# Performance work log

Measured on AMD Instinct MI355X. Metric: run time of the kernel, lower is better.

The kernel has to match this reference:

```python
import jax, jax.numpy as jnp
import numpy as np


def setup_inputs() -> dict:
    key = jax.random.key(0)
    ks = jax.random.split(key, 5)
    B, H, W, KV = 32, 32, 32, 1024
    N, K, V = 16, 64, 64
    return {
        "key_value": jax.random.normal(ks[0], (B, H, W, KV), dtype=jnp.float32),
        "query": jax.random.normal(ks[1], (1, 1, N, K), dtype=jnp.float32),
        "k_kernel": jax.random.normal(ks[2], (KV, N * K), dtype=jnp.float32) * 0.03,
        "k_bias": jnp.zeros((N * K,), dtype=jnp.float32),
        "v_kernel": jax.random.normal(ks[3], (KV, N * V), dtype=jnp.float32) * 0.03,
        "v_bias": jnp.zeros((N * V,), dtype=jnp.float32),
    }


def reference(key_value, query, k_kernel, k_bias, v_kernel, v_bias):
    # key_value: [B,H,W,KV]; 1x1 conv == channel GEMM
    B, H, W, KV = key_value.shape
    N, K = query.shape[2], query.shape[3]
    V = v_kernel.shape[1] // N
    x = key_value.reshape(B, H * W, KV)                      # [B,HW,KV]
    k = (x @ k_kernel + k_bias).reshape(B, H * W, N, K)       # [B,HW,N,K]
    v = (x @ v_kernel + v_bias).reshape(B, H * W, N, V)       # [B,HW,N,V]
    # single-query dot product per head (no 1/sqrt(K) scaling, per original)
    logits = jnp.einsum('bsnk,nk->bsn', k, query[0, 0])       # [B,HW,N]
    attn = jax.nn.softmax(logits, axis=1)                     # softmax over HW
    out = jnp.einsum('bsn,bsnv->bnv', attn, v)                # [B,N,V]
    return out
```

## Files before the change

### kernel.cpp

```cpp
#include <hip/hip_runtime.h>
#include <hip/hip_fp16.h>


__device__ __forceinline__ float rlane(float v, int l) {
  return __int_as_float(__builtin_amdgcn_readlane(__float_as_int(v), l));
}

__global__ __launch_bounds__(256) void k_qk(const float* __restrict__ kk,
                                            const float* __restrict__ q,
                                            const float* __restrict__ kb,
                                            __half* __restrict__ qkh,
                                            float* __restrict__ qb) {
  const int gid = blockIdx.x * 256 + threadIdx.x;
  const int c = gid >> 4, n = gid & 15;
  float a = 0.f;
#pragma unroll
  for (int k4 = 0; k4 < 64; k4 += 4) {
    const float4 kv = *(const float4*)(kk + (size_t)c * 1024 + n * 64 + k4);
    const float4 qv = *(const float4*)(q + n * 64 + k4);
    a += kv.x * qv.x + kv.y * qv.y + kv.z * qv.z + kv.w * qv.w;
  }
  qkh[(n >> 2) * 4096 + c * 4 + (n & 3)] = __float2half(a);
  if (blockIdx.x == 0 && threadIdx.x < 16) {
    float s = 0.f;
    for (int k = 0; k < 64; k++) s += kb[threadIdx.x * 64 + k] * q[threadIdx.x * 64 + k];
    qb[threadIdx.x] = s;
  }
}

__global__ __launch_bounds__(512, 4) void k_fused(const float* __restrict__ x,
                                                  const __half* __restrict__ qkh,
                                                  const float* __restrict__ qb,
                                                  float* __restrict__ mch,
                                                  float* __restrict__ lch,
                                                  __half* __restrict__ wph) {
  __shared__ uint2 qkt[4096];
  __shared__ float et2[64 * 17 + 4];
  const int tid = threadIdx.x;
  const int lane = tid & 63;
  const int wid = tid >> 6;
  const int blk = blockIdx.x;
  const int srow0 = blk * 64;

  {
    const uint4* src = (const uint4*)qkh;
#pragma unroll
    for (int it = 0; it < 4; ++it) {
      const int g = it * 512 + tid;
      ((uint4*)qkt)[g] = src[g];
    }
  }
  __syncthreads();

#pragma unroll 1
  for (int sweep = 0; sweep < 2; ++sweep) {
    const int rloc = sweep * 32 + wid * 4;
    const float* xw = x + (size_t)(srow0 + rloc) * 1024 + lane;

    float acc[4][16];
#pragma unroll
    for (int r = 0; r < 4; ++r)
#pragma unroll
      for (int n = 0; n < 16; ++n) acc[r][n] = 0.f;

    float xa[4], xb[4];
#pragma unroll
    for (int r = 0; r < 4; ++r) xa[r] = xw[(size_t)r * 1024];

#pragma unroll 1
    for (int st = 0; st < 16; st += 2) {
#pragma unroll
      for (int r = 0; r < 4; ++r) xb[r] = xw[(size_t)r * 1024 + (st + 1) * 64];
      {
        const int c = st * 64 + lane;
#pragma unroll
        for (int nq = 0; nq < 4; ++nq) {
          const uint2 hv = qkt[nq * 1024 + c];
          const float2 f01 = __half22float2(*(const __half2*)&hv.x);
          const float2 f23 = __half22float2(*(const __half2*)&hv.y);
#pragma unroll
          for (int r = 0; r < 4; ++r) {
            acc[r][nq * 4 + 0] += xa[r] * f01.x;
            acc[r][nq * 4 + 1] += xa[r] * f01.y;
            acc[r][nq * 4 + 2] += xa[r] * f23.x;
            acc[r][nq * 4 + 3] += xa[r] * f23.y;
          }
        }
      }
      if (st + 2 < 16) {
#pragma unroll
        for (int r = 0; r < 4; ++r) xa[r] = xw[(size_t)r * 1024 + (st + 2) * 64];
      }
      {
        const int c = (st + 1) * 64 + lane;
#pragma unroll
        for (int nq = 0; nq < 4; ++nq) {
          const uint2 hv = qkt[nq * 1024 + c];
          const float2 f01 = __half22float2(*(const __half2*)&hv.x);
          const float2 f23 = __half22float2(*(const __half2*)&hv.y);
#pragma unroll
          for (int r = 0; r < 4; ++r) {
            acc[r][nq * 4 + 0] += xb[r] * f01.x;
            acc[r][nq * 4 + 1] += xb[r] * f01.y;
            acc[r][nq * 4 + 2] += xb[r] * f23.x;
            acc[r][nq * 4 + 3] += xb[r] * f23.y;
          }
        }
      }
    }

    const int b0 = lane & 1, b1 = (lane >> 1) & 1;
    const int b2 = (lane >> 2) & 1, b3 = (lane >> 3) & 1;
    float f[4];
#pragma unroll
    for (int r = 0; r < 4; ++r) {
      float u[8];
#pragma unroll
      for (int m = 0; m < 8; ++m) {
        const float keep = b0 ? acc[r][2 * m + 1] : acc[r][2 * m];
        const float give = b0 ? acc[r][2 * m]     : acc[r][2 * m + 1];
        u[m] = keep + __shfl_xor(give, 1);
      }
      float w[4];
#pragma unroll
      for (int p = 0; p < 4; ++p) {
        const float keep = b1 ? u[2 * p + 1] : u[2 * p];
        const float give = b1 ? u[2 * p]     : u[2 * p + 1];
        w[p] = keep + __shfl_xor(give, 2);
      }
      float z[2];
#pragma unroll
      for (int qq = 0; qq < 2; ++qq) {
        const float keep = b2 ? w[2 * qq + 1] : w[2 * qq];
        const float give = b2 ? w[2 * qq]     : w[2 * qq + 1];
        z[qq] = keep + __shfl_xor(give, 4);
      }
      {
        const float keep = b3 ? z[1] : z[0];
        const float give = b3 ? z[0] : z[1];
        float t = keep + __shfl_xor(give, 8);
        t += __shfl_xor(t, 16);
        t += __shfl_xor(t, 32);
        f[r] = t;
      }
    }
    const int rsel = lane >> 4;
    float val = (rsel == 0) ? f[0] : (rsel == 1) ? f[1] : (rsel == 2) ? f[2] : f[3];
    val += qb[lane & 15];
    et2[(rloc + rsel) * 17 + (lane & 15)] = val;
  }
  __syncthreads();

#pragma unroll
  for (int t = 0; t < 2; ++t) {
    const int nn = wid + t * 8;
    const float v = et2[lane * 17 + nn];
    float m = v;
#pragma unroll
    for (int d = 1; d < 64; d <<= 1) m = fmaxf(m, __shfl_xor(m, d));
    const float e = __expf(v - m);
    float s = e;
#pragma unroll
    for (int d = 1; d < 64; d <<= 1) s += __shfl_xor(s, d);
    if (lane == 0) {
      mch[blk * 16 + nn] = m;
      lch[blk * 16 + nn] = s;
    }
    et2[lane * 17 + nn] = e;
  }
  __syncthreads();

  {
    const int c0 = tid * 2;
    float acc0[16], acc1[16];
#pragma unroll
    for (int n = 0; n < 16; ++n) { acc0[n] = 0.f; acc1[n] = 0.f; }
    const float* xp = x + (size_t)srow0 * 1024 + c0;

    float  ea = et2[(lane >> 4) * 17 + (lane & 15)];
    float2 xca[4];
#pragma unroll
    for (int ss = 0; ss < 4; ++ss) xca[ss] = *(const float2*)(xp + (size_t)ss * 1024);

#pragma unroll 1
    for (int sg = 0; sg < 16; ++sg) {
      float  eb = 0.f;
      float2 xcb[4];
      if (sg < 15) {
        const int s0n = (sg + 1) * 4;
        eb = et2[(s0n + (lane >> 4)) * 17 + (lane & 15)];
#pragma unroll
        for (int ss = 0; ss < 4; ++ss)
          xcb[ss] = *(const float2*)(xp + (size_t)(s0n + ss) * 1024);
      }
#pragma unroll
      for (int ss = 0; ss < 4; ++ss) {
#pragma unroll
        for (int n = 0; n < 16; ++n) {
          const float ev = rlane(ea, ss * 16 + n);
          acc0[n] += ev * xca[ss].x;
          acc1[n] += ev * xca[ss].y;
        }
      }
      ea = eb;
#pragma unroll
      for (int ss = 0; ss < 4; ++ss) xca[ss] = xcb[ss];
    }

    __half* wpp = wph + (size_t)blk * 16384;
#pragma unroll
    for (int n = 0; n < 16; ++n) {
      __half2 h = __floats2half2_rn(acc0[n], acc1[n]);
      *(__half2*)(wpp + n * 1024 + c0) = h;
    }
  }
}

__global__ __launch_bounds__(256) void k_out(const __half* __restrict__ wph,
                                             const float* __restrict__ vk,
                                             const float* __restrict__ vb,
                                             const float* __restrict__ mch,
                                             const float* __restrict__ lch,
                                             float* __restrict__ out) {
  const int bi = blockIdx.x;
  const int b = bi >> 4, n = bi & 15;
  const int tid = threadIdx.x;
  __shared__ float wrow[1024];
  __shared__ float red[4][64];

  float m16[16], l16[16];
#pragma unroll
  for (int ch = 0; ch < 16; ++ch) {
    m16[ch] = mch[(b * 16 + ch) * 16 + n];
    l16[ch] = lch[(b * 16 + ch) * 16 + n];
  }
  float mg = m16[0];
#pragma unroll
  for (int ch = 1; ch < 16; ++ch) mg = fmaxf(mg, m16[ch]);
  float fac[16], lg = 0.f;
#pragma unroll
  for (int ch = 0; ch < 16; ++ch) { fac[ch] = __expf(m16[ch] - mg); lg += fac[ch] * l16[ch]; }

  float4 a4 = {0.f, 0.f, 0.f, 0.f};
#pragma unroll
  for (int ch = 0; ch < 16; ch++) {
    const __half2* p = (const __half2*)(wph + ((size_t)(b * 16 + ch) * 16 + n) * 1024 + tid * 4);
    const float2 f01 = __half22float2(p[0]);
    const float2 f23 = __half22float2(p[1]);
    a4.x += fac[ch] * f01.x; a4.y += fac[ch] * f01.y;
    a4.z += fac[ch] * f23.x; a4.w += fac[ch] * f23.y;
  }
  *(float4*)&wrow[tid * 4] = a4;
  __syncthreads();

  const int v = tid & 63, cq = tid >> 6;
  float a = 0.f;
  const float* vkc = vk + n * 64 + v;
  for (int ci = 0; ci < 256; ci++) {
    const int c = cq * 256 + ci;
    a += wrow[c] * vkc[(size_t)c * 1024];
  }
  red[cq][v] = a;
  __syncthreads();
  if (tid < 64) {
    const float o = (red[0][tid] + red[1][tid] + red[2][tid] + red[3][tid]) / lg
                    + vb[n * 64 + tid];
    out[(size_t)b * 1024 + n * 64 + tid] = o;
  }
}

extern "C" void kernel_launch(void* const* d_in, const int* in_sizes, int n_in,
                              void* d_out, int out_size, void* d_ws, size_t ws_size,
                              hipStream_t stream) {
  const float* x  = (const float*)d_in[0];
  const float* q  = (const float*)d_in[1];
  const float* kk = (const float*)d_in[2];
  const float* kb = (const float*)d_in[3];
  const float* vk = (const float*)d_in[4];
  const float* vb = (const float*)d_in[5];
  float* out = (float*)d_out;

  float*  f   = (float*)d_ws;
  __half* qkh = (__half*)f;
  float*  qb  = f + 8192;
  float*  mch = f + 8208;
  float*  lch = f + 16400;
  __half* wph = (__half*)(f + 24592);

  hipLaunchKernelGGL(k_qk,    dim3(64),  dim3(256), 0, stream, kk, q, kb, qkh, qb);
  hipLaunchKernelGGL(k_fused, dim3(512), dim3(512), 0, stream, x, qkh, qb, mch, lch, wph);
  hipLaunchKernelGGL(k_out,   dim3(512), dim3(256), 0, stream, wph, vk, vb, mch, lch, out);
}
```

Baseline: 69.25 us.

## Compute logits GEMM with fp16 MFMA instead of scalar FMA loops

Replaces the scalar FP32 FMA accumulation of x·(Wk q) in the fused kernel with 16x16x32 f16 MFMA instructions. The qk vector is stored in a blocked layout that matches the MFMA B operand, and x is converted to fp16 on the fly. The K dimension is split across two wave halves, whose partial results are summed through shared memory, and the long shuffle-reduction tree is removed. This lowers ALU and LDS work in the logit stage, but x is now rounded to fp16, which costs some accuracy, and two extra block barriers are added.

Result: faster. 66.98 us (-3.3%).

```diff
diff --git a/kernel.cpp b/kernel.cpp
--- a/kernel.cpp
+++ b/kernel.cpp
@@ -1,6 +1,9 @@
 #include <hip/hip_runtime.h>
 #include <hip/hip_fp16.h>
 
+
+typedef _Float16 f16x8 __attribute__((ext_vector_type(8)));
+typedef float f32x4 __attribute__((ext_vector_type(4)));
 
 __device__ __forceinline__ float rlane(float v, int l) {
   return __int_as_float(__builtin_amdgcn_readlane(__float_as_int(v), l));
@@ -9,7 +12,7 @@
 __global__ __launch_bounds__(256) void k_qk(const float* __restrict__ kk,
                                             const float* __restrict__ q,
                                             const float* __restrict__ kb,
-                                            __half* __restrict__ qkh,
+                                            __half* __restrict__ qkb,
                                             float* __restrict__ qb) {
   const int gid = blockIdx.x * 256 + threadIdx.x;
   const int c = gid >> 4, n = gid & 15;
@@ -20,7 +23,10 @@
     const float4 qv = *(const float4*)(q + n * 64 + k4);
     a += kv.x * qv.x + kv.y * qv.y + kv.z * qv.z + kv.w * qv.w;
   }
-  qkh[(n >> 2) * 4096 + c * 4 + (n & 3)] = __float2half(a);
+  const int kbi = c >> 5;
+  const int l = (((c >> 3) & 3) << 4) | n;
+  const int j = c & 7;
+  qkb[kbi * 512 + l * 8 + j] = __float2half(a);
   if (blockIdx.x == 0 && threadIdx.x < 16) {
     float s = 0.f;
     for (int k = 0; k < 64; k++) s += kb[threadIdx.x * 64 + k] * q[threadIdx.x * 64 + k];
@@ -29,12 +35,12 @@
 }
 
 __global__ __launch_bounds__(512, 4) void k_fused(const float* __restrict__ x,
-                                                  const __half* __restrict__ qkh,
+                                                  const __half* __restrict__ qkb,
                                                   const float* __restrict__ qb,
                                                   float* __restrict__ mch,
                                                   float* __restrict__ lch,
                                                   __half* __restrict__ wph) {
-  __shared__ uint2 qkt[4096];
+  __shared__ __half qkt[16384];
   __shared__ float et2[64 * 17 + 4];
   const int tid = threadIdx.x;
   const int lane = tid & 63;
@@ -42,114 +48,69 @@
   const int blk = blockIdx.x;
   const int srow0 = blk * 64;
 
+#pragma unroll
+  for (int it = 0; it < 4; ++it) {
+    const int g = it * 512 + tid;
+    ((uint4*)qkt)[g] = ((const uint4*)qkb)[g];
+  }
+  __syncthreads();
+
   {
-    const uint4* src = (const uint4*)qkh;
-#pragma unroll
-    for (int it = 0; it < 4; ++it) {
-      const int g = it * 512 + tid;
-      ((uint4*)qkt)[g] = src[g];
-    }
-  }
-  __syncthreads();
+    const int wtile = wid & 3;
+    const int khalf = wid >> 2;
+    const int r16 = lane & 15;
+    const int khi = lane >> 4;
+    const float* xg = x + (size_t)(srow0 + wtile * 16 + r16) * 1024
+                        + khalf * 512 + khi * 8;
+    const __half* qbase = qkt + (khalf * 16) * 512 + lane * 8;
+
+    f32x4 dacc = {0.f, 0.f, 0.f, 0.f};
+    float4 pa0 = *(const float4*)(xg);
+    float4 pa1 = *(const float4*)(xg + 4);
+    float4 pb0, pb1;
 
 #pragma unroll 1
-  for (int sweep = 0; sweep < 2; ++sweep) {
-    const int rloc = sweep * 32 + wid * 4;
-    const float* xw = x + (size_t)(srow0 + rloc) * 1024 + lane;
-
-    float acc[4][16];
-#pragma unroll
-    for (int r = 0; r < 4; ++r)
-#pragma unroll
-      for (int n = 0; n < 16; ++n) acc[r][n] = 0.f;
-
-    float xa[4], xb[4];
-#pragma unroll
-    for (int r = 0; r < 4; ++r) xa[r] = xw[(size_t)r * 1024];
-
-#pragma unroll 1
-    for (int st = 0; st < 16; st += 2) {
-#pragma unroll
-      for (int r = 0; r < 4; ++r) xb[r] = xw[(size_t)r * 1024 + (st + 1) * 64];
+    for (int kbs = 0; kbs < 16; kbs += 2) {
+      pb0 = *(const float4*)(xg + (kbs + 1) * 32);
+      pb1 = *(const float4*)(xg + (kbs + 1) * 32 + 4);
       {
-        const int c = st * 64 + lane;
-#pragma unroll
-        for (int nq = 0; nq < 4; ++nq) {
-          const uint2 hv = qkt[nq * 1024 + c];
-          const float2 f01 = __half22float2(*(const __half2*)&hv.x);
-          const float2 f23 = __half22float2(*(const __half2*)&hv.y);
-#pragma unroll
-          for (int r = 0; r < 4; ++r) {
-            acc[r][nq * 4 + 0] += xa[r] * f01.x;
-            acc[r][nq * 4 + 1] += xa[r] * f01.y;
-            acc[r][nq * 4 + 2] += xa[r] * f23.x;
-            acc[r][nq * 4 + 3] += xa[r] * f23.y;
-          }
-        }
-      }
-      if (st + 2 < 16) {
-#pragma unroll
-        for (int r = 0; r < 4; ++r) xa[r] = xw[(size_t)r * 1024 + (st + 2) * 64];
+        f16x8 af;
+        af[0] = (_Float16)pa0.x; af[1] = (_Float16)pa0.y;
+        af[2] = (_Float16)pa0.z; af[3] = (_Float16)pa0.w;
+        af[4] = (_Float16)pa1.x; af[5] = (_Float16)pa1.y;
+        af[6] = (_Float16)pa1.z; af[7] = (_Float16)pa1.w;
+        const f16x8 bf = *(const f16x8*)(qbase + kbs * 512);
+        dacc = __builtin_amdgcn_mfma_f32_16x16x32_f16(af, bf, dacc, 0, 0, 0);
+      }
+      if (kbs + 2 < 16) {
+        pa0 = *(const float4*)(xg + (kbs + 2) * 32);
+        pa1 = *(const float4*)(xg + (kbs + 2) * 32 + 4);
       }
       {
-        const int c = (st + 1) * 64 + lane;
-#pragma unroll
-        for (int nq = 0; nq < 4; ++nq) {
-          const uint2 hv = qkt[nq * 1024 + c];
-          const float2 f01 = __half22float2(*(const __half2*)&hv.x);
-          const float2 f23 = __half22float2(*(const __half2*)&hv.y);
-#pragma unroll
-          for (int r = 0; r < 4; ++r) {
-            acc[r][nq * 4 + 0] += xb[r] * f01.x;
-            acc[r][nq * 4 + 1] += xb[r] * f01.y;
-            acc[r][nq * 4 + 2] += xb[r] * f23.x;
-            acc[r][nq * 4 + 3] += xb[r] * f23.y;
-          }
-        }
-      }
-    }
-
-    const int b0 = lane & 1, b1 = (lane >> 1) & 1;
-    const int b2 = (lane >> 2) & 1, b3 = (lane >> 3) & 1;
-    float f[4];
-#pragma unroll
-    for (int r = 0; r < 4; ++r) {
-      float u[8];
-#pragma unroll
-      for (int m = 0; m < 8; ++m) {
-        const float keep = b0 ? acc[r][2 * m + 1] : acc[r][2 * m];
-        const float give = b0 ? acc[r][2 * m]     : acc[r][2 * m + 1];
-        u[m] = keep + __shfl_xor(give, 1);
-      }
-      float w[4];
-#pragma unroll
-      for (int p = 0; p < 4; ++p) {
-        const float keep = b1 ? u[2 * p + 1] : u[2 * p];
-        const float give = b1 ? u[2 * p]     : u[2 * p + 1];
-        w[p] = keep + __shfl_xor(give, 2);
-      }
-      float z[2];
-#pragma unroll
-      for (int qq = 0; qq < 2; ++qq) {
-        const float keep = b2 ? w[2 * qq + 1] : w[2 * qq];
-        const float give = b2 ? w[2 * qq]     : w[2 * qq + 1];
-        z[qq] = keep + __shfl_xor(give, 4);
-      }
-      {
-        const float keep = b3 ? z[1] : z[0];
-        const float give = b3 ? z[0] : z[1];
-        float t = keep + __shfl_xor(give, 8);
-        t += __shfl_xor(t, 16);
-        t += __shfl_xor(t, 32);
-        f[r] = t;
-      }
-    }
-    const int rsel = lane >> 4;
-    float val = (rsel == 0) ? f[0] : (rsel == 1) ? f[1] : (rsel == 2) ? f[2] : f[3];
-    val += qb[lane & 15];
-    et2[(rloc + rsel) * 17 + (lane & 15)] = val;
-  }
-  __syncthreads();
+        f16x8 af;
+        af[0] = (_Float16)pb0.x; af[1] = (_Float16)pb0.y;
+        af[2] = (_Float16)pb0.z; af[3] = (_Float16)pb0.w;
+        af[4] = (_Float16)pb1.x; af[5] = (_Float16)pb1.y;
+        af[6] = (_Float16)pb1.z; af[7] = (_Float16)pb1.w;
+        const f16x8 bf = *(const f16x8*)(qbase + (kbs + 1) * 512);
+        dacc = __builtin_amdgcn_mfma_f32_16x16x32_f16(af, bf, dacc, 0, 0, 0);
+      }
+    }
+
+    const float qbv = qb[r16];
+    if (khalf == 0) {
+#pragma unroll
+      for (int reg = 0; reg < 4; ++reg)
+        et2[(wtile * 16 + khi * 4 + reg) * 17 + r16] = dacc[reg] + qbv;
+    }
+    __syncthreads();
+    if (khalf == 1) {
+#pragma unroll
+      for (int reg = 0; reg < 4; ++reg)
+        et2[(wtile * 16 + khi * 4 + reg) * 17 + r16] += dacc[reg];
+    }
+    __syncthreads();
+  }
 
 #pragma unroll
   for (int t = 0; t < 2; ++t) {
@@ -281,13 +242,13 @@
   float* out = (float*)d_out;
 
   float*  f   = (float*)d_ws;
-  __half* qkh = (__half*)f;
+  __half* qkb = (__half*)f;
   float*  qb  = f + 8192;
   float*  mch = f + 8208;
   float*  lch = f + 16400;
   __half* wph = (__half*)(f + 24592);
 
-  hipLaunchKernelGGL(k_qk,    dim3(64),  dim3(256), 0, stream, kk, q, kb, qkh, qb);
-  hipLaunchKernelGGL(k_fused, dim3(512), dim3(512), 0, stream, x, qkh, qb, mch, lch, wph);
+  hipLaunchKernelGGL(k_qk,    dim3(64),  dim3(256), 0, stream, kk, q, kb, qkb, qb);
+  hipLaunchKernelGGL(k_fused, dim3(512), dim3(512), 0, stream, x, qkb, qb, mch, lch, wph);
   hipLaunchKernelGGL(k_out,   dim3(512), dim3(256), 0, stream, wph, vk, vb, mch, lch, out);
 }
```
